# Performance work log

Hardware: AMD Instinct MI355X
Metric: run time of the kernel (lower is better)

## Reference

```python
import jax, jax.numpy as jnp
import numpy as np

B, S, DM = 1, 2048, 1024
H, D, T = 16, 64, 16
NA = 3  # anchor tiles per query (local tile appended -> 4 tiles, 64 tokens)


def setup_inputs() -> dict:
    key = jax.random.key(0)
    ks = jax.random.split(key, 6)
    sc = 1.0 / np.sqrt(DM)
    x = jax.random.normal(ks[0], (B, S, DM), jnp.float32)
    Wq = jax.random.normal(ks[1], (DM, H * D), jnp.float32) * sc
    Wk = jax.random.normal(ks[2], (DM, H * D), jnp.float32) * sc
    Wv = jax.random.normal(ks[3], (DM, H * D), jnp.float32) * sc
    Wo = jax.random.normal(ks[4], (H * D, DM), jnp.float32) * sc
    anchor_indices = jax.random.randint(ks[5], (B, H, S, NA), 0, S // T).astype(jnp.int32)
    # RoPE freqs: freqs_cis[s, j] = exp(i * s * theta_j), half-split convention
    half = D // 2
    inv_freq = 1.0 / (10000.0 ** (np.arange(half, dtype=np.float64) / half))
    ang = np.outer(np.arange(S), inv_freq)  # [S, half]
    cos = jnp.asarray(np.cos(ang), jnp.float32)
    sin = jnp.asarray(np.sin(ang), jnp.float32)
    return {"x": x, "Wq": Wq, "Wk": Wk, "Wv": Wv, "Wo": Wo,
            "cos": cos, "sin": sin, "anchor_indices": anchor_indices}


def _rotate_half(z):
    h = z.shape[-1] // 2
    return jnp.concatenate([-z[..., h:], z[..., :h]], axis=-1)


def reference(x, Wq, Wk, Wv, Wo, cos, sin, anchor_indices):
    b, s, _ = x.shape
    # projections -> [B, H, S, D]
    q = (x @ Wq).reshape(b, s, H, D).transpose(0, 2, 1, 3)
    k = (x @ Wk).reshape(b, s, H, D).transpose(0, 2, 1, 3)
    v = (x @ Wv).reshape(b, s, H, D).transpose(0, 2, 1, 3)
    # RoPE (half-split / rotate_half)
    cos_f = jnp.concatenate([cos, cos], axis=-1)[None, None]  # [1,1,S,D]
    sin_f = jnp.concatenate([sin, sin], axis=-1)[None, None]
    q = q * cos_f + _rotate_half(q) * sin_f
    k = k * cos_f + _rotate_half(k) * sin_f
    # tile index set: anchor tiles + local tile
    local = (jnp.arange(s) // T).astype(jnp.int32)
    local = jnp.broadcast_to(local[None, None, :, None], (b, H, s, 1))
    tiles = jnp.concatenate([anchor_indices, local], axis=-1)  # [B,H,S,NA+1]
    tok = tiles[..., None] * T + jnp.arange(T, dtype=jnp.int32)  # [B,H,S,NA+1,T]
    K = (NA + 1) * T  # sparse_len
    idx = jnp.clip(tok.reshape(b, H, s, K), 0, s - 1)
    # per-(b,h) per-query gather of K/V -> [B,H,S,K,D]
    gather = jax.vmap(jax.vmap(lambda kv, i: kv[i]))
    k_sp = gather(k, idx)
    v_sp = gather(v, idx)
    logits = jnp.einsum('bhqd,bhqkd->bhqk', q, k_sp) / jnp.sqrt(jnp.float32(D))
    qidx = jnp.arange(s)[None, None, :, None]
    fut = idx > qidx  # causal mask over gathered keys
    logits = jnp.where(fut, -1e10, logits)
    w = jax.nn.softmax(logits, axis=-1)
    fully_masked = jnp.all(fut, axis=-1, keepdims=True)
    w = jnp.where(fully_masked, 0.0, w)
    w = jnp.where(jnp.isnan(w), 0.0, w)
    out = jnp.einsum('bhqk,bhqkd->bhqd', w, v_sp)
    out = out.transpose(0, 2, 1, 3).reshape(b, s, H * D)
    return out @ Wo
```

## Files before the change

### kernel.cpp

```cpp
#include <hip/hip_runtime.h>
#include <hip/hip_bf16.h>


#define S_LEN 2048
#define DM 1024
#define NH 16
#define HD 64
#define LDK 40

typedef __bf16 bf16x8 __attribute__((ext_vector_type(8)));
typedef float f32x4 __attribute__((ext_vector_type(4)));

static __device__ __forceinline__ unsigned short f2bf(float f) {
    union { float f; unsigned int i; } un;
    un.f = f;
    unsigned int r = un.i + 0x7FFFu + ((un.i >> 16) & 1u);
    return (unsigned short)(r >> 16);
}
static __device__ __forceinline__ float bfu2f(unsigned short u) {
    union { unsigned int i; float f; } un;
    un.i = ((unsigned int)u) << 16;
    return un.f;
}
static __device__ __forceinline__ float bflo(unsigned int u) {
    union { unsigned int i; float f; } un;
    un.i = u << 16;
    return un.f;
}
static __device__ __forceinline__ float bfhi(unsigned int u) {
    union { unsigned int i; float f; } un;
    un.i = u & 0xFFFF0000u;
    return un.f;
}

__global__ __launch_bounds__(256) void conv_x(
    const float* __restrict__ x, unsigned short* __restrict__ xb) {
    int i = (blockIdx.x * 256 + threadIdx.x) * 4;
    float4 f = *(const float4*)(x + i);
    ushort4 o;
    o.x = f2bf(f.x); o.y = f2bf(f.y); o.z = f2bf(f.z); o.w = f2bf(f.w);
    *(ushort4*)(xb + i) = o;
}

__global__ __launch_bounds__(256) void trans_w(
    const float* __restrict__ W0, const float* __restrict__ W1,
    const float* __restrict__ W2, const float* __restrict__ W3,
    unsigned short* __restrict__ T0, unsigned short* __restrict__ T1,
    unsigned short* __restrict__ T2, unsigned short* __restrict__ T3) {
    const int z = blockIdx.z;
    const float* W = (z == 0) ? W0 : (z == 1) ? W1 : (z == 2) ? W2 : W3;
    unsigned short* T = (z == 0) ? T0 : (z == 1) ? T1 : (z == 2) ? T2 : T3;
    __shared__ float t[32][33];
    const int bn = blockIdx.x * 32, bk = blockIdx.y * 32;
    const int tx = threadIdx.x & 31, ty = threadIdx.x >> 5;
    #pragma unroll
    for (int m = 0; m < 4; ++m)
        t[ty + m * 8][tx] = W[(size_t)(bk + ty + m * 8) * 1024 + bn + tx];
    __syncthreads();
    #pragma unroll
    for (int m = 0; m < 4; ++m)
        T[(size_t)(bn + ty + m * 8) * 1024 + bk + tx] = f2bf(t[tx][ty + m * 8]);
}

__global__ __launch_bounds__(256) void gemm_qkv(
    const unsigned short* __restrict__ xb,
    const unsigned short* __restrict__ Wtq, const unsigned short* __restrict__ Wtk,
    const unsigned short* __restrict__ Wtv,
    unsigned short* __restrict__ qh, unsigned short* __restrict__ kh,
    unsigned short* __restrict__ vh,
    const float* __restrict__ cs, const float* __restrict__ sn) {
    __shared__ __align__(16) unsigned short Al[128 * LDK];
    __shared__ __align__(16) unsigned short Bl[128 * LDK];
    const int tid = threadIdx.x;
    const int nb = blockIdx.x >> 3;
    const unsigned short* __restrict__ Bt = (nb == 0) ? Wtq : (nb == 1) ? Wtk : Wtv;
    unsigned short* __restrict__ OUT = (nb == 0) ? qh : (nb == 1) ? kh : vh;
    const int col0 = (blockIdx.x & 7) * 128;
    const int row0 = blockIdx.y * 128;
    const int lane = tid & 63, wvi = tid >> 6;
    const int wr = (wvi >> 1) * 64, wc = (wvi & 1) * 64;
    const int l15 = lane & 15, quad = lane >> 4;
    const int srow = tid >> 1, skq = (tid & 1) << 4;

    f32x4 acc[4][4] = {};
    for (int k0 = 0; k0 < 1024; k0 += 32) {
        const unsigned short* ga = xb + (size_t)(row0 + srow) * 1024 + k0 + skq;
        uint4 a0 = *(const uint4*)ga;
        uint4 a1 = *(const uint4*)(ga + 8);
        const unsigned short* gb = Bt + (size_t)(col0 + srow) * 1024 + k0 + skq;
        uint4 b0 = *(const uint4*)gb;
        uint4 b1 = *(const uint4*)(gb + 8);
        __syncthreads();
        unsigned short* ad = &Al[srow * LDK + skq];
        *(uint4*)ad = a0; *(uint4*)(ad + 8) = a1;
        unsigned short* bd = &Bl[srow * LDK + skq];
        *(uint4*)bd = b0; *(uint4*)(bd + 8) = b1;
        __syncthreads();
        bf16x8 af[4], bfr[4];
        #pragma unroll
        for (int i = 0; i < 4; ++i)
            af[i] = *(const bf16x8*)&Al[(wr + i * 16 + l15) * LDK + quad * 8];
        #pragma unroll
        for (int j = 0; j < 4; ++j)
            bfr[j] = *(const bf16x8*)&Bl[(wc + j * 16 + l15) * LDK + quad * 8];
        #pragma unroll
        for (int i = 0; i < 4; ++i)
            #pragma unroll
            for (int j = 0; j < 4; ++j)
                acc[i][j] = __builtin_amdgcn_mfma_f32_16x16x32_bf16(
                    af[i], bfr[j], acc[i][j], 0, 0, 0);
    }

    const int hh = ((blockIdx.x & 7) << 1) + (wc >> 6);
    const bool dorope = (nb != 2);
    #pragma unroll
    for (int i = 0; i < 4; ++i) {
        const int rowb = row0 + wr + i * 16 + quad * 4;
        #pragma unroll
        for (int r = 0; r < 4; ++r) {
            const int s = rowb + r;
            float v0 = acc[i][0][r], v1 = acc[i][1][r];
            float v2 = acc[i][2][r], v3 = acc[i][3][r];
            if (dorope) {
                float c0 = cs[s * 32 + l15],      s0 = sn[s * 32 + l15];
                float c1 = cs[s * 32 + 16 + l15], s1 = sn[s * 32 + 16 + l15];
                float lo0 = v0 * c0 - v2 * s0;
                float hi0 = v2 * c0 + v0 * s0;
                float lo1 = v1 * c1 - v3 * s1;
                float hi1 = v3 * c1 + v1 * s1;
                v0 = lo0; v1 = lo1; v2 = hi0; v3 = hi1;
            }
            unsigned short* op = OUT + (size_t)hh * (S_LEN * 64) + (size_t)s * 64 + l15;
            op[0]  = f2bf(v0);
            op[16] = f2bf(v1);
            op[32] = f2bf(v2);
            op[48] = f2bf(v3);
        }
    }
}

__global__ __launch_bounds__(256) void attn_kernel(
    const unsigned short* __restrict__ qh, const unsigned short* __restrict__ kh,
    const unsigned short* __restrict__ vh, const int* __restrict__ anc,
    unsigned short* __restrict__ att) {
    __shared__ __align__(16) float qs[4][64];
    __shared__ __align__(16) int   ts[4][64];
    __shared__ __align__(16) float ws[4][64];
    const int w4 = threadIdx.x >> 6;
    const int lane = threadIdx.x & 63;
    const int wid = (blockIdx.x << 2) + w4;
    const int h = wid >> 11;
    const int qi = wid & 2047;
    const size_t hb = (size_t)h * (S_LEN * 64);

    const float q_own = bfu2f(qh[hb + (size_t)qi * 64 + lane]);
    const int slot = lane >> 4;
    const int tile = (slot < 3) ? anc[((size_t)h * S_LEN + qi) * 3 + slot]
                                : (qi >> 4);
    const int tok_own = tile * 16 + (lane & 15);
    qs[w4][lane] = q_own;
    ts[w4][lane] = tok_own;

    const int c = lane & 3;
    const int t = lane >> 2;
    float qv[16];
    #pragma unroll
    for (int r = 0; r < 4; ++r) {
        float4 f = *(const float4*)&qs[w4][c * 16 + r * 4];
        qv[r * 4 + 0] = f.x; qv[r * 4 + 1] = f.y;
        qv[r * 4 + 2] = f.z; qv[r * 4 + 3] = f.w;
    }

    #pragma unroll
    for (int p = 0; p < 4; ++p) {
        const int tk = ts[w4][p * 16 + t];
        const unsigned short* kp = kh + hb + (size_t)tk * 64 + c * 16;
        const uint4 k0 = *(const uint4*)kp;
        const uint4 k1 = *(const uint4*)(kp + 8);
        float part;
        part = bflo(k0.x) * qv[0];
        part = fmaf(bfhi(k0.x), qv[1], part);
        part = fmaf(bflo(k0.y), qv[2], part);
        part = fmaf(bfhi(k0.y), qv[3], part);
        part = fmaf(bflo(k0.z), qv[4], part);
        part = fmaf(bfhi(k0.z), qv[5], part);
        part = fmaf(bflo(k0.w), qv[6], part);
        part = fmaf(bfhi(k0.w), qv[7], part);
        part = fmaf(bflo(k1.x), qv[8], part);
        part = fmaf(bfhi(k1.x), qv[9], part);
        part = fmaf(bflo(k1.y), qv[10], part);
        part = fmaf(bfhi(k1.y), qv[11], part);
        part = fmaf(bflo(k1.z), qv[12], part);
        part = fmaf(bfhi(k1.z), qv[13], part);
        part = fmaf(bflo(k1.w), qv[14], part);
        part = fmaf(bfhi(k1.w), qv[15], part);
        part += __shfl_xor(part, 1, 64);
        part += __shfl_xor(part, 2, 64);
        if (c == 0) ws[w4][p * 16 + t] = part;
    }

    float logit = ws[w4][lane];
    const bool fut = tok_own > qi;
    logit = fut ? -1e30f : logit * 0.125f;

    float m = logit;
    #pragma unroll
    for (int off = 32; off >= 1; off >>= 1)
        m = fmaxf(m, __shfl_xor(m, off, 64));
    const float e = fut ? 0.f : __expf(logit - m);
    float ssum = e;
    #pragma unroll
    for (int off = 32; off >= 1; off >>= 1)
        ssum += __shfl_xor(ssum, off, 64);
    ws[w4][lane] = e / ssum;

    float out = 0.f;
    #pragma unroll
    for (int kk = 0; kk < 64; kk += 8) {
        float w8[8]; int t8[8];
        *(float4*)&w8[0] = *(const float4*)&ws[w4][kk];
        *(float4*)&w8[4] = *(const float4*)&ws[w4][kk + 4];
        *(int4*)&t8[0]   = *(const int4*)&ts[w4][kk];
        *(int4*)&t8[4]   = *(const int4*)&ts[w4][kk + 4];
        float vv[8];
        #pragma unroll
        for (int j = 0; j < 8; ++j)
            vv[j] = bfu2f(vh[hb + (size_t)t8[j] * 64 + lane]);
        #pragma unroll
        for (int j = 0; j < 8; ++j)
            out = fmaf(w8[j], vv[j], out);
    }
    att[(size_t)qi * DM + h * HD + lane] = f2bf(out);
}

__global__ __launch_bounds__(256) void gemm_out(
    const unsigned short* __restrict__ A, const unsigned short* __restrict__ Bt,
    float* __restrict__ C) {
    __shared__ __align__(16) unsigned short Al[64 * LDK];
    __shared__ __align__(16) unsigned short Bl[128 * LDK];
    const int tid = threadIdx.x;
    const int col0 = blockIdx.x * 128;
    const int row0 = blockIdx.y * 64;
    const int lane = tid & 63, wvi = tid >> 6;
    const int wr = (wvi >> 1) * 32, wc = (wvi & 1) * 64;
    const int l15 = lane & 15, quad = lane >> 4;
    const int rowA = tid >> 2, kqA = (tid & 3) << 3;
    const int rowB = tid >> 1, kqB = (tid & 1) << 4;

    f32x4 acc[2][4] = {};
    for (int k0 = 0; k0 < 1024; k0 += 32) {
        const uint4 a0 = *(const uint4*)(A + (size_t)(row0 + rowA) * 1024 + k0 + kqA);
        const unsigned short* gb = Bt + (size_t)(col0 + rowB) * 1024 + k0 + kqB;
        const uint4 b0 = *(const uint4*)gb;
        const uint4 b1 = *(const uint4*)(gb + 8);
        __syncthreads();
        *(uint4*)&Al[rowA * LDK + kqA] = a0;
        unsigned short* bd = &Bl[rowB * LDK + kqB];
        *(uint4*)bd = b0; *(uint4*)(bd + 8) = b1;
        __syncthreads();
        bf16x8 af[2], bfr[4];
        #pragma unroll
        for (int i = 0; i < 2; ++i)
            af[i] = *(const bf16x8*)&Al[(wr + i * 16 + l15) * LDK + quad * 8];
        #pragma unroll
        for (int j = 0; j < 4; ++j)
            bfr[j] = *(const bf16x8*)&Bl[(wc + j * 16 + l15) * LDK + quad * 8];
        #pragma unroll
        for (int i = 0; i < 2; ++i)
            #pragma unroll
            for (int j = 0; j < 4; ++j)
                acc[i][j] = __builtin_amdgcn_mfma_f32_16x16x32_bf16(
                    af[i], bfr[j], acc[i][j], 0, 0, 0);
    }
    #pragma unroll
    for (int i = 0; i < 2; ++i) {
        const int rowb = row0 + wr + i * 16 + quad * 4;
        #pragma unroll
        for (int r = 0; r < 4; ++r) {
            float* crow = C + (size_t)(rowb + r) * 1024 + col0 + wc;
            #pragma unroll
            for (int j = 0; j < 4; ++j)
                crow[j * 16 + l15] = acc[i][j][r];
        }
    }
}

extern "C" void kernel_launch(void* const* d_in, const int* in_sizes, int n_in,
                              void* d_out, int out_size, void* d_ws, size_t ws_size,
                              hipStream_t stream) {
    const float* x   = (const float*)d_in[0];
    const float* Wq  = (const float*)d_in[1];
    const float* Wk  = (const float*)d_in[2];
    const float* Wv  = (const float*)d_in[3];
    const float* Wo  = (const float*)d_in[4];
    const float* cs  = (const float*)d_in[5];
    const float* sn  = (const float*)d_in[6];
    const int*   anc = (const int*)d_in[7];
    float* out = (float*)d_out;

    unsigned short* xb  = (unsigned short*)d_ws;
    unsigned short* Wtq = xb  + (size_t)2048 * 1024;
    unsigned short* Wtk = Wtq + (size_t)1024 * 1024;
    unsigned short* Wtv = Wtk + (size_t)1024 * 1024;
    unsigned short* Wto = Wtv + (size_t)1024 * 1024;
    unsigned short* qh  = Wto + (size_t)1024 * 1024;
    unsigned short* kh  = qh  + (size_t)2048 * 1024;
    unsigned short* vh  = kh  + (size_t)2048 * 1024;
    unsigned short* att = vh  + (size_t)2048 * 1024;

    conv_x<<<2048, 256, 0, stream>>>(x, xb);
    trans_w<<<dim3(32, 32, 4), 256, 0, stream>>>(Wq, Wk, Wv, Wo,
                                                 Wtq, Wtk, Wtv, Wto);
    gemm_qkv<<<dim3(24, 16), 256, 0, stream>>>(xb, Wtq, Wtk, Wtv,
                                               qh, kh, vh, cs, sn);
    attn_kernel<<<(S_LEN * NH) / 4, 256, 0, stream>>>(qh, kh, vh, anc, att);
    gemm_out<<<dim3(8, 32), 256, 0, stream>>>(att, Wto, out);
}
```

Measured before the change: 165.1 us.

## Merge prep kernels, shrink QKV GEMM row tile, pack attention weights with indices

Combines the x conversion and the weight transposes into one prep launch, which removes a kernel launch. Halves the QKV GEMM row tile to 64 so the grid has 768 blocks instead of 384, giving better occupancy across the CUs. In attention, each softmax weight is rounded to bf16 and packed with its token index into one 32-bit word, which halves the LDS reads in the V accumulation loop. The cost is a small precision loss on the weights and more global reloads of the B tile in the GEMM.

```diff
diff --git a/kernel.cpp b/kernel.cpp
--- a/kernel.cpp
+++ b/kernel.cpp
@@ -33,33 +33,37 @@
     return un.f;
 }
 
-__global__ __launch_bounds__(256) void conv_x(
-    const float* __restrict__ x, unsigned short* __restrict__ xb) {
-    int i = (blockIdx.x * 256 + threadIdx.x) * 4;
-    float4 f = *(const float4*)(x + i);
-    ushort4 o;
-    o.x = f2bf(f.x); o.y = f2bf(f.y); o.z = f2bf(f.z); o.w = f2bf(f.w);
-    *(ushort4*)(xb + i) = o;
-}
-
-__global__ __launch_bounds__(256) void trans_w(
+__global__ __launch_bounds__(256) void prep(
+    const float* __restrict__ x, unsigned short* __restrict__ xb,
     const float* __restrict__ W0, const float* __restrict__ W1,
     const float* __restrict__ W2, const float* __restrict__ W3,
     unsigned short* __restrict__ T0, unsigned short* __restrict__ T1,
     unsigned short* __restrict__ T2, unsigned short* __restrict__ T3) {
-    const int z = blockIdx.z;
-    const float* W = (z == 0) ? W0 : (z == 1) ? W1 : (z == 2) ? W2 : W3;
-    unsigned short* T = (z == 0) ? T0 : (z == 1) ? T1 : (z == 2) ? T2 : T3;
-    __shared__ float t[32][33];
-    const int bn = blockIdx.x * 32, bk = blockIdx.y * 32;
-    const int tx = threadIdx.x & 31, ty = threadIdx.x >> 5;
-    #pragma unroll
-    for (int m = 0; m < 4; ++m)
-        t[ty + m * 8][tx] = W[(size_t)(bk + ty + m * 8) * 1024 + bn + tx];
-    __syncthreads();
-    #pragma unroll
-    for (int m = 0; m < 4; ++m)
-        T[(size_t)(bn + ty + m * 8) * 1024 + bk + tx] = f2bf(t[tx][ty + m * 8]);
+    const int bx = blockIdx.x;
+    if (bx < 4096) {
+        const int z = bx >> 10, rem = bx & 1023;
+        const float* W = (z == 0) ? W0 : (z == 1) ? W1 : (z == 2) ? W2 : W3;
+        unsigned short* T = (z == 0) ? T0 : (z == 1) ? T1 : (z == 2) ? T2 : T3;
+        __shared__ float t[32][33];
+        const int bn = (rem & 31) * 32, bk = (rem >> 5) * 32;
+        const int tx = threadIdx.x & 31, ty = threadIdx.x >> 5;
+        #pragma unroll
+        for (int m = 0; m < 4; ++m)
+            t[ty + m * 8][tx] = W[(size_t)(bk + ty + m * 8) * 1024 + bn + tx];
+        __syncthreads();
+        #pragma unroll
+        for (int m = 0; m < 4; ++m)
+            T[(size_t)(bn + ty + m * 8) * 1024 + bk + tx] = f2bf(t[tx][ty + m * 8]);
+    } else {
+        const int i = (bx - 4096) * 2048 + threadIdx.x * 8;
+        float4 f0 = *(const float4*)(x + i);
+        float4 f1 = *(const float4*)(x + i + 4);
+        ushort4 o0, o1;
+        o0.x = f2bf(f0.x); o0.y = f2bf(f0.y); o0.z = f2bf(f0.z); o0.w = f2bf(f0.w);
+        o1.x = f2bf(f1.x); o1.y = f2bf(f1.y); o1.z = f2bf(f1.z); o1.w = f2bf(f1.w);
+        *(ushort4*)(xb + i) = o0;
+        *(ushort4*)(xb + i + 4) = o1;
+    }
 }
 
 __global__ __launch_bounds__(256) void gemm_qkv(
@@ -69,42 +73,40 @@
     unsigned short* __restrict__ qh, unsigned short* __restrict__ kh,
     unsigned short* __restrict__ vh,
     const float* __restrict__ cs, const float* __restrict__ sn) {
-    __shared__ __align__(16) unsigned short Al[128 * LDK];
+    __shared__ __align__(16) unsigned short Al[64 * LDK];
     __shared__ __align__(16) unsigned short Bl[128 * LDK];
     const int tid = threadIdx.x;
     const int nb = blockIdx.x >> 3;
     const unsigned short* __restrict__ Bt = (nb == 0) ? Wtq : (nb == 1) ? Wtk : Wtv;
     unsigned short* __restrict__ OUT = (nb == 0) ? qh : (nb == 1) ? kh : vh;
     const int col0 = (blockIdx.x & 7) * 128;
-    const int row0 = blockIdx.y * 128;
+    const int row0 = blockIdx.y * 64;
     const int lane = tid & 63, wvi = tid >> 6;
-    const int wr = (wvi >> 1) * 64, wc = (wvi & 1) * 64;
+    const int wr = (wvi >> 1) * 32, wc = (wvi & 1) * 64;
     const int l15 = lane & 15, quad = lane >> 4;
-    const int srow = tid >> 1, skq = (tid & 1) << 4;
-
-    f32x4 acc[4][4] = {};
+    const int rowA = tid >> 2, kqA = (tid & 3) << 3;
+    const int rowB = tid >> 1, kqB = (tid & 1) << 4;
+
+    f32x4 acc[2][4] = {};
     for (int k0 = 0; k0 < 1024; k0 += 32) {
-        const unsigned short* ga = xb + (size_t)(row0 + srow) * 1024 + k0 + skq;
-        uint4 a0 = *(const uint4*)ga;
-        uint4 a1 = *(const uint4*)(ga + 8);
-        const unsigned short* gb = Bt + (size_t)(col0 + srow) * 1024 + k0 + skq;
-        uint4 b0 = *(const uint4*)gb;
-        uint4 b1 = *(const uint4*)(gb + 8);
-        __syncthreads();
-        unsigned short* ad = &Al[srow * LDK + skq];
-        *(uint4*)ad = a0; *(uint4*)(ad + 8) = a1;
-        unsigned short* bd = &Bl[srow * LDK + skq];
+        const uint4 a0 = *(const uint4*)(xb + (size_t)(row0 + rowA) * 1024 + k0 + kqA);
+        const unsigned short* gb = Bt + (size_t)(col0 + rowB) * 1024 + k0 + kqB;
+        const uint4 b0 = *(const uint4*)gb;
+        const uint4 b1 = *(const uint4*)(gb + 8);
+        __syncthreads();
+        *(uint4*)&Al[rowA * LDK + kqA] = a0;
+        unsigned short* bd = &Bl[rowB * LDK + kqB];
         *(uint4*)bd = b0; *(uint4*)(bd + 8) = b1;
         __syncthreads();
-        bf16x8 af[4], bfr[4];
-        #pragma unroll
-        for (int i = 0; i < 4; ++i)
+        bf16x8 af[2], bfr[4];
+        #pragma unroll
+        for (int i = 0; i < 2; ++i)
             af[i] = *(const bf16x8*)&Al[(wr + i * 16 + l15) * LDK + quad * 8];
         #pragma unroll
         for (int j = 0; j < 4; ++j)
             bfr[j] = *(const bf16x8*)&Bl[(wc + j * 16 + l15) * LDK + quad * 8];
         #pragma unroll
-        for (int i = 0; i < 4; ++i)
+        for (int i = 0; i < 2; ++i)
             #pragma unroll
             for (int j = 0; j < 4; ++j)
                 acc[i][j] = __builtin_amdgcn_mfma_f32_16x16x32_bf16(
@@ -114,7 +116,7 @@
     const int hh = ((blockIdx.x & 7) << 1) + (wc >> 6);
     const bool dorope = (nb != 2);
     #pragma unroll
-    for (int i = 0; i < 4; ++i) {
+    for (int i = 0; i < 2; ++i) {
         const int rowb = row0 + wr + i * 16 + quad * 4;
         #pragma unroll
         for (int r = 0; r < 4; ++r) {
@@ -146,6 +148,7 @@
     __shared__ __align__(16) float qs[4][64];
     __shared__ __align__(16) int   ts[4][64];
     __shared__ __align__(16) float ws[4][64];
+    __shared__ __align__(16) unsigned int ps[4][64];
     const int w4 = threadIdx.x >> 6;
     const int lane = threadIdx.x & 63;
     const int wid = (blockIdx.x << 2) + w4;
@@ -212,23 +215,22 @@
     #pragma unroll
     for (int off = 32; off >= 1; off >>= 1)
         ssum += __shfl_xor(ssum, off, 64);
-    ws[w4][lane] = e / ssum;
+    ps[w4][lane] = ((unsigned int)tok_own << 16) | f2bf(e / ssum);
 
     float out = 0.f;
     #pragma unroll
     for (int kk = 0; kk < 64; kk += 8) {
-        float w8[8]; int t8[8];
-        *(float4*)&w8[0] = *(const float4*)&ws[w4][kk];
-        *(float4*)&w8[4] = *(const float4*)&ws[w4][kk + 4];
-        *(int4*)&t8[0]   = *(const int4*)&ts[w4][kk];
-        *(int4*)&t8[4]   = *(const int4*)&ts[w4][kk + 4];
+        const uint4 pa = *(const uint4*)&ps[w4][kk];
+        const uint4 pb = *(const uint4*)&ps[w4][kk + 4];
+        const unsigned int p8[8] = {pa.x, pa.y, pa.z, pa.w,
+                                    pb.x, pb.y, pb.z, pb.w};
         float vv[8];
         #pragma unroll
         for (int j = 0; j < 8; ++j)
-            vv[j] = bfu2f(vh[hb + (size_t)t8[j] * 64 + lane]);
+            vv[j] = bfu2f(vh[hb + (size_t)(p8[j] >> 16) * 64 + lane]);
         #pragma unroll
         for (int j = 0; j < 8; ++j)
-            out = fmaf(w8[j], vv[j], out);
+            out = fmaf(bflo(p8[j]), vv[j], out);
     }
     att[(size_t)qi * DM + h * HD + lane] = f2bf(out);
 }
@@ -308,10 +310,8 @@
     unsigned short* vh  = kh  + (size_t)2048 * 1024;
     unsigned short* att = vh  + (size_t)2048 * 1024;
 
-    conv_x<<<2048, 256, 0, stream>>>(x, xb);
-    trans_w<<<dim3(32, 32, 4), 256, 0, stream>>>(Wq, Wk, Wv, Wo,
-                                                 Wtq, Wtk, Wtv, Wto);
-    gemm_qkv<<<dim3(24, 16), 256, 0, stream>>>(xb, Wtq, Wtk, Wtv,
+    prep<<<5120, 256, 0, stream>>>(x, xb, Wq, Wk, Wv, Wo, Wtq, Wtk, Wtv, Wto);
+    gemm_qkv<<<dim3(24, 32), 256, 0, stream>>>(xb, Wtq, Wtk, Wtv,
                                                qh, kh, vh, cs, sn);
     attn_kernel<<<(S_LEN * NH) / 4, 256, 0, stream>>>(qh, kh, vh, anc, att);
     gemm_out<<<dim3(8, 32), 256, 0, stream>>>(att, Wto, out);
```

After: 207.3 us. 25.6% more time.
